# Performance work log

Measured on AMD Instinct MI355X. Metric: run time of the kernel, lower is better.

The kernel has to match this reference:

```python
import jax, jax.numpy as jnp
import numpy as np

K = 20
EPS = 1e-5


def _bn(x, g, b):
    # inference-mode BatchNorm with running_mean=0, running_var=1 (fresh init)
    return x * (g / jnp.sqrt(1.0 + EPS)) + b


def _lrelu(x):
    return jax.nn.leaky_relu(x, 0.2)


def _knn(x, k):
    # x: [B,N,D] -> idx [B,N,k] of nearest neighbors (includes self)
    sq = jnp.sum(x * x, axis=-1)                       # [B,N]
    inner = jnp.einsum('bnd,bmd->bnm', x, x)           # [B,N,N]
    dist = sq[:, :, None] - 2.0 * inner + sq[:, None, :]
    _, idx = jax.lax.top_k(-dist, k)
    return idx


def _edge_feat(x, k):
    # x: [B,N,D] -> [B,N,k,2D] = concat(neighbor - center, center)
    idx = _knn(x, k)
    nbr = jax.vmap(lambda xb, ib: xb[ib])(x, idx)      # [B,N,k,D]
    ctr = jnp.broadcast_to(x[:, :, None, :], nbr.shape)
    return jnp.concatenate([nbr - ctr, ctr], axis=-1)


def _edge_conv(x, W, g, b, k):
    # conv1x1 (no bias) + BN + LeakyReLU + max over neighbors
    f = _edge_feat(x, k)                               # [B,N,k,2D]
    h = jnp.einsum('bnkc,oc->bnko', f, W)
    return jnp.max(_lrelu(_bn(h, g, b)), axis=2)       # [B,N,out]


def setup_inputs() -> dict:
    key = jax.random.key(0)
    ks = jax.random.split(key, 12)
    B, N = 8, 4096
    num_classes = 5
    r = lambda k_, shape: jax.random.normal(k_, shape, jnp.float32) * 0.1
    return {
        'xyz': jax.random.normal(ks[0], (B, N, 3), jnp.float32),
        'W1': r(ks[1], (64, 6)),   'g1': jnp.ones((64,), jnp.float32),  'b1': jnp.zeros((64,), jnp.float32),
        'W2': r(ks[2], (64, 128)), 'g2': jnp.ones((64,), jnp.float32),  'b2': jnp.zeros((64,), jnp.float32),
        'W3': r(ks[3], (64, 128)), 'g3': jnp.ones((64,), jnp.float32),  'b3': jnp.zeros((64,), jnp.float32),
        'W4': r(ks[4], (128, 128)),'g4': jnp.ones((128,), jnp.float32), 'b4': jnp.zeros((128,), jnp.float32),
        'W5': r(ks[5], (1024, 320)),'g5': jnp.ones((1024,), jnp.float32),'b5': jnp.zeros((1024,), jnp.float32),
        'Wl1': r(ks[6], (512, 2048)),'g6': jnp.ones((512,), jnp.float32),'b6': jnp.zeros((512,), jnp.float32),
        'Wl2': r(ks[7], (256, 512)), 'bl2': jnp.zeros((256,), jnp.float32),
        'g7': jnp.ones((256,), jnp.float32), 'b7': jnp.zeros((256,), jnp.float32),
        'Wl3': r(ks[8], (num_classes, 256)), 'bl3': jnp.zeros((num_classes,), jnp.float32),
    }


def reference(xyz, W1, g1, b1, W2, g2, b2, W3, g3, b3, W4, g4, b4,
              W5, g5, b5, Wl1, g6, b6, Wl2, bl2, g7, b7, Wl3, bl3):
    B, N, _ = xyz.shape
    k = min(K, N - 1)
    x1 = _edge_conv(xyz, W1, g1, b1, k)                # [B,N,64]
    x2 = _edge_conv(x1, W2, g2, b2, k)                 # [B,N,64]
    x3 = _edge_conv(x2, W3, g3, b3, k)                 # [B,N,64]
    x4 = _edge_conv(x3, W4, g4, b4, k)                 # [B,N,128]
    xc = jnp.concatenate([x1, x2, x3, x4], axis=-1)    # [B,N,320]
    h = _lrelu(_bn(jnp.einsum('bnc,oc->bno', xc, W5), g5, b5))  # [B,N,1024]
    gmax = jnp.max(h, axis=1)
    gavg = jnp.mean(h, axis=1)
    gfeat = jnp.concatenate([gmax, gavg], axis=-1)     # [B,2048]
    y = _lrelu(_bn(gfeat @ Wl1.T, g6, b6))             # dropout = identity (eval)
    y = _lrelu(_bn(y @ Wl2.T + bl2, g7, b7))
    y = y @ Wl3.T + bl3                                # [B,num_classes]
    return jnp.broadcast_to(y[:, None, :], (B, N, y.shape[-1]))
```

## Files before the change

### kernel.cpp

```cpp
#include <hip/hip_runtime.h>


constexpr int NB  = 8;
constexpr int NPT = 4096;
constexpr int KNB = 20;

typedef _Float16 half8 __attribute__((ext_vector_type(8)));
typedef float f32x4 __attribute__((ext_vector_type(4)));

__device__ __forceinline__ unsigned int fmono(float f) {
  unsigned int u = __float_as_uint(f);
  return u ^ ((unsigned int)(((int)u) >> 31) | 0x80000000u);
}

__device__ __attribute__((noinline)) unsigned long long sort_row(int row, int n,
                                                                 int lane) {
  extern __shared__ char smem[];
  unsigned long long* buf = (unsigned long long*)smem + (size_t)row * 64;
  const unsigned long long INFK = ~0ull;
  unsigned long long a = (lane < n) ? buf[lane] : INFK;
#pragma unroll
  for (int k = 2; k <= 64; k <<= 1) {
#pragma unroll
    for (int j = k >> 1; j > 0; j >>= 1) {
      const bool tm = (((lane & k) == 0) == ((lane & j) == 0));
      const unsigned long long oa = __shfl_xor(a, j, 64);
      a = ((a < oa) == tm) ? a : oa;
    }
  }
  if (lane < 20) buf[lane] = a;
  return a;
}

__device__ __forceinline__ void sel_q(unsigned long long key, int base_r,
                                      int quad, int l15, int lane,
                                      unsigned long long& tau_r, int& cnt_r) {
  extern __shared__ char smem[];
  unsigned long long* bufB = (unsigned long long*)smem;
  bool pass = key < tau_r;
  unsigned long long m = __ballot(pass);
  if (m == 0) return;
  unsigned int seg = (unsigned int)(m >> (quad * 16)) & 0xFFFFu;
  int pc = __popc(seg);
  const unsigned long long needm = __ballot(cnt_r + pc > 64);
  if (needm != 0) {
#pragma unroll
    for (int q = 0; q < 4; ++q) {
      if ((needm >> (q * 16)) & 1ull) {
        const int nq = __shfl(cnt_r, q * 16, 64);
        const unsigned long long sv = sort_row(base_r + q * 4, nq, lane);
        const unsigned long long t19 = __shfl(sv, 19, 64);
        if (quad == q) { tau_r = t19; cnt_r = 20; }
      }
    }
    pass = key < tau_r;
    m = __ballot(pass);
    seg = (unsigned int)(m >> (quad * 16)) & 0xFFFFu;
    pc = __popc(seg);
  }
  if (pass) {
    const int off = __popc(seg & ((1u << l15) - 1u));
    bufB[(size_t)(base_r + quad * 4) * 64 + cnt_r + off] = key;
  }
  cnt_r += pc;
}

__global__ __launch_bounds__(256) void cvt_xyz(const float* __restrict__ xyz,
                                               float* __restrict__ x0) {
  const int t = blockIdx.x * 256 + threadIdx.x;
  float4 v;
  v.x = xyz[t * 3 + 0];
  v.y = xyz[t * 3 + 1];
  v.z = xyz[t * 3 + 2];
  v.w = 0.0f;
  *(float4*)(x0 + (size_t)t * 4) = v;
}

__global__ __launch_bounds__(256) void sqsplit(const float* __restrict__ x,
                                               float* __restrict__ sqo,
                                               unsigned short* __restrict__ xhi,
                                               unsigned short* __restrict__ xlo) {
  const int t = blockIdx.x * 256 + threadIdx.x;
  const int p = t >> 2, c = t & 3;
  const float* src = x + (size_t)p * 64 + c * 16;
  float s = 0.0f;
  unsigned short hb[16], lb[16];
#pragma unroll
  for (int e = 0; e < 16; e += 4) {
    const float4 v = *(const float4*)(src + e);
    const float vv[4] = {v.x, v.y, v.z, v.w};
#pragma unroll
    for (int u = 0; u < 4; ++u) {
      const float f = vv[u];
      s = fmaf(f, f, s);
      const _Float16 h = (_Float16)f;
      const _Float16 l = (_Float16)(f - (float)h);
      hb[e + u] = __builtin_bit_cast(unsigned short, h);
      lb[e + u] = __builtin_bit_cast(unsigned short, l);
    }
  }
  unsigned short* dh = xhi + (size_t)p * 64 + c * 16;
  unsigned short* dl = xlo + (size_t)p * 64 + c * 16;
  *(uint4*)dh = *(uint4*)hb;
  *(uint4*)(dh + 8) = *(uint4*)(hb + 8);
  *(uint4*)dl = *(uint4*)lb;
  *(uint4*)(dl + 8) = *(uint4*)(lb + 8);
  s += __shfl_xor(s, 1, 64);
  s += __shfl_xor(s, 2, 64);
  if (c == 0) sqo[p] = s;
}

__global__ __launch_bounds__(256, 4) void knn3(const float* __restrict__ x0,
                                               int* __restrict__ idxout) {
  const int b = blockIdx.y, i0 = blockIdx.x * 64;
  const int tid = threadIdx.x, w = tid >> 6, lane = tid & 63;
  const int l15 = lane & 15, quad = lane >> 4;
  const float* xb = x0 + (size_t)b * (NPT * 4);

  float xix[4], xiy[4], xiz[4];
#pragma unroll
  for (int r = 0; r < 4; ++r) {
    const float4 v =
        *(const float4*)(xb + (size_t)(i0 + w * 16 + quad * 4 + r) * 4);
    xix[r] = v.x;
    xiy[r] = v.y;
    xiz[r] = v.z;
  }

  unsigned long long tau[4] = {~0ull, ~0ull, ~0ull, ~0ull};
  int cnt[4] = {0, 0, 0, 0};

  for (int jt = 0; jt < NPT / 64; ++jt) {
    const int j0 = jt * 64;
    float4 xj[4];
#pragma unroll
    for (int nj = 0; nj < 4; ++nj)
      xj[nj] = *(const float4*)(xb + (size_t)(j0 + nj * 16 + l15) * 4);
#pragma unroll
    for (int r = 0; r < 4; ++r) {
#pragma unroll
      for (int nj = 0; nj < 4; ++nj) {
        const float dx = xj[nj].x - xix[r];
        const float dy = xj[nj].y - xiy[r];
        const float dz = xj[nj].z - xiz[r];
        const float dd = fmaf(dx, dx, fmaf(dy, dy, dz * dz));
        const unsigned long long key =
            ((unsigned long long)fmono(dd) << 32) |
            (unsigned int)(j0 + nj * 16 + l15);
        sel_q(key, w * 16 + r, quad, l15, lane, tau[r], cnt[r]);
      }
    }
  }
#pragma unroll
  for (int rw = 0; rw < 16; ++rw) {
    const int q = rw >> 2, r = rw & 3;
    const int nq = __shfl(cnt[r], q * 16, 64);
    const unsigned long long sv = sort_row(w * 16 + rw, nq, lane);
    const int i = i0 + w * 16 + rw;
    if (lane < 20)
      idxout[((size_t)(b * NPT + i)) * KNB + lane] = (int)(unsigned int)sv;
  }
}

__global__ __launch_bounds__(256, 4) void knn_mfma(
    const unsigned short* __restrict__ xhi16,
    const unsigned short* __restrict__ xlo16,
    const float* __restrict__ sqn, int* __restrict__ idxout) {
  const int b = blockIdx.y, i0 = blockIdx.x * 64;
  const int tid = threadIdx.x, w = tid >> 6, lane = tid & 63;
  const int l15 = lane & 15, quad = lane >> 4;

  const half8* Hb = (const half8*)(xhi16 + (size_t)b * NPT * 64);
  const half8* Lb = (const half8*)(xlo16 + (size_t)b * NPT * 64);
  const float* sqb = sqn + b * NPT;

  const int ia = i0 + w * 16 + l15;
  const half8 ah0 = Hb[(size_t)ia * 8 + quad];
  const half8 ah1 = Hb[(size_t)ia * 8 + 4 + quad];
  const half8 al0 = Lb[(size_t)ia * 8 + quad];
  const half8 al1 = Lb[(size_t)ia * 8 + 4 + quad];

  unsigned long long tau[4] = {~0ull, ~0ull, ~0ull, ~0ull};
  int cnt[4] = {0, 0, 0, 0};

  for (int jt = 0; jt < NPT / 64; ++jt) {
    const int j0 = jt * 64;
    float sq4[4];
#pragma unroll
    for (int nj = 0; nj < 4; ++nj) sq4[nj] = sqb[j0 + nj * 16 + l15];
    f32x4 acc[4];
#pragma unroll
    for (int nj = 0; nj < 4; ++nj) {
      const int jb = j0 + nj * 16 + l15;
      const half8 bh0 = Hb[(size_t)jb * 8 + quad];
      const half8 bh1 = Hb[(size_t)jb * 8 + 4 + quad];
      const half8 bl0 = Lb[(size_t)jb * 8 + quad];
      const half8 bl1 = Lb[(size_t)jb * 8 + 4 + quad];
      f32x4 a = {0.0f, 0.0f, 0.0f, 0.0f};
      a = __builtin_amdgcn_mfma_f32_16x16x32_f16(al0, bh0, a, 0, 0, 0);
      a = __builtin_amdgcn_mfma_f32_16x16x32_f16(al1, bh1, a, 0, 0, 0);
      a = __builtin_amdgcn_mfma_f32_16x16x32_f16(ah0, bl0, a, 0, 0, 0);
      a = __builtin_amdgcn_mfma_f32_16x16x32_f16(ah1, bl1, a, 0, 0, 0);
      a = __builtin_amdgcn_mfma_f32_16x16x32_f16(ah0, bh0, a, 0, 0, 0);
      a = __builtin_amdgcn_mfma_f32_16x16x32_f16(ah1, bh1, a, 0, 0, 0);
      acc[nj] = a;
    }
#pragma unroll
    for (int r = 0; r < 4; ++r) {
#pragma unroll
      for (int nj = 0; nj < 4; ++nj) {
        const float dd = fmaf(-2.0f, acc[nj][r], sq4[nj]);
        const unsigned long long key =
            ((unsigned long long)fmono(dd) << 32) |
            (unsigned int)(j0 + nj * 16 + l15);
        sel_q(key, w * 16 + r, quad, l15, lane, tau[r], cnt[r]);
      }
    }
  }
#pragma unroll
  for (int rw = 0; rw < 16; ++rw) {
    const int q = rw >> 2, r = rw & 3;
    const int nq = __shfl(cnt[r], q * 16, 64);
    const unsigned long long sv = sort_row(w * 16 + rw, nq, lane);
    const int i = i0 + w * 16 + rw;
    if (lane < 20)
      idxout[((size_t)(b * NPT + i)) * KNB + lane] = (int)(unsigned int)sv;
  }
}

__global__ __launch_bounds__(256) void featg3(const float* __restrict__ x0,
                                              const float* __restrict__ W,
                                              float* __restrict__ Y) {
  const int lane = threadIdx.x & 63;
  const int p0 = (blockIdx.x * 4 + (threadIdx.x >> 6)) * 4;
  const float* wr = W + lane * 6;
  const float w0 = wr[0], w1 = wr[1], w2 = wr[2];
#pragma unroll
  for (int r = 0; r < 4; ++r) {
    const float4 v = *(const float4*)(x0 + (size_t)(p0 + r) * 4);
    Y[(size_t)(p0 + r) * 64 + lane] = w0 * v.x + w1 * v.y + w2 * v.z;
  }
}

__global__ __launch_bounds__(256) void featg64(const float* __restrict__ X,
                                               const float* __restrict__ W,
                                               int co, float* __restrict__ Y) {
  __shared__ float Xt[64][68];
  __shared__ float Wt[64][68];
  const int tid = threadIdx.x;
  const int n0 = blockIdx.x * 64;
  const int pc = tid & 63, dg = tid >> 6;
#pragma unroll
  for (int rep = 0; rep < 4; ++rep) {
    const int d0 = dg * 16 + rep * 4;
    const float4 xv = *(const float4*)(X + (size_t)(n0 + pc) * 64 + d0);
    Xt[d0 + 0][pc] = xv.x; Xt[d0 + 1][pc] = xv.y;
    Xt[d0 + 2][pc] = xv.z; Xt[d0 + 3][pc] = xv.w;
    const float4 wv = *(const float4*)(W + (size_t)(co + pc) * 128 + d0);
    Wt[d0 + 0][pc] = wv.x; Wt[d0 + 1][pc] = wv.y;
    Wt[d0 + 2][pc] = wv.z; Wt[d0 + 3][pc] = wv.w;
  }
  __syncthreads();
  const int c0 = (tid & 15) * 4, p0 = (tid >> 4) * 4;
  float acc[4][4];
#pragma unroll
  for (int i = 0; i < 4; ++i)
#pragma unroll
    for (int j = 0; j < 4; ++j) acc[i][j] = 0.0f;
#pragma unroll 4
  for (int d = 0; d < 64; ++d) {
    const float4 xa = *(const float4*)&Xt[d][p0];
    const float4 wc = *(const float4*)&Wt[d][c0];
    const float xr[4] = {xa.x, xa.y, xa.z, xa.w};
    const float wr[4] = {wc.x, wc.y, wc.z, wc.w};
#pragma unroll
    for (int i = 0; i < 4; ++i)
#pragma unroll
      for (int j = 0; j < 4; ++j) acc[i][j] = fmaf(xr[i], wr[j], acc[i][j]);
  }
#pragma unroll
  for (int i = 0; i < 4; ++i) {
    float4 o;
    o.x = acc[i][0]; o.y = acc[i][1]; o.z = acc[i][2]; o.w = acc[i][3];
    *(float4*)(Y + (size_t)(n0 + p0 + i) * 64 + c0) = o;
  }
}

template <int DIN, int DS, int COUT>
__global__ __launch_bounds__(256) void gather_edge(
    const float* __restrict__ x, const float* __restrict__ Y,
    const int* __restrict__ idx, const float* __restrict__ W,
    const float* __restrict__ g, const float* __restrict__ bia,
    float* __restrict__ out, int co) {
  const int lane = threadIdx.x & 63;
  const int wglob = blockIdx.x * 4 + (threadIdx.x >> 6);
  const int b = wglob >> 12;
  const int c = co + lane;

  const float* wrow = W + (size_t)c * (2 * DIN);
  const float* xi = x + (size_t)wglob * DS;
  float Dv = 0.0f;
  if constexpr (DIN == 3) {
    const float4 v = *(const float4*)xi;
    Dv = (wrow[3] - wrow[0]) * v.x + (wrow[4] - wrow[1]) * v.y +
         (wrow[5] - wrow[2]) * v.z;
  } else {
#pragma unroll
    for (int d0 = 0; d0 < DIN; d0 += 4) {
      const float4 wa4 = *(const float4*)(wrow + d0);
      const float4 wb4 = *(const float4*)(wrow + DIN + d0);
      const float4 v = *(const float4*)(xi + d0);
      Dv += (wb4.x - wa4.x) * v.x + (wb4.y - wa4.y) * v.y +
            (wb4.z - wa4.z) * v.z + (wb4.w - wa4.w) * v.w;
    }
  }
  const float invs = 1.0f / sqrtf(1.0f + 1e-5f);
  const float s = g[c] * invs;
  const float base = fmaf(s, Dv, bia[c]);

  const int* ip = idx + (size_t)wglob * KNB;
  const int jv = ip[lane < KNB ? lane : 0];
  const float* Yb = Y + (((size_t)b) << 12) * 64;
  float m = -3.0e38f;
#pragma unroll
  for (int k = 0; k < KNB; ++k) {
    const int j = __shfl(jv, k, 64);
    const float yv = Yb[(size_t)j * 64 + lane];
    float v = fmaf(s, yv, base);
    v = v > 0.0f ? v : 0.2f * v;
    m = fmaxf(m, v);
  }
  out[(size_t)wglob * COUT + c] = m;
}

__global__ __launch_bounds__(256) void conv5_kernel(
    const float* __restrict__ x1, const float* __restrict__ x2,
    const float* __restrict__ x3, const float* __restrict__ x4,
    const float* __restrict__ W5, const float* __restrict__ g5,
    const float* __restrict__ b5, float* __restrict__ pmax,
    float* __restrict__ psum) {
  __shared__ float xcT[320][32];
  __shared__ float wT[8][256];
  const int nb = blockIdx.x, cb = blockIdx.y, b = blockIdx.z;
  const int tid = threadIdx.x;
  const int n0 = nb * 32;

#pragma unroll
  for (int p = 0; p < 10; ++p) {
    const int q = tid + p * 256;
    const int nloc = q / 80;
    const int kg = (q % 80) * 4;
    const float* src;
    int koff;
    if (kg < 64)       { src = x1 + ((size_t)(b * NPT + n0 + nloc)) * 64;  koff = kg; }
    else if (kg < 128) { src = x2 + ((size_t)(b * NPT + n0 + nloc)) * 64;  koff = kg - 64; }
    else if (kg < 192) { src = x3 + ((size_t)(b * NPT + n0 + nloc)) * 64;  koff = kg - 128; }
    else               { src = x4 + ((size_t)(b * NPT + n0 + nloc)) * 128; koff = kg - 192; }
    const float4 v = *(const float4*)(src + koff);
    xcT[kg + 0][nloc] = v.x; xcT[kg + 1][nloc] = v.y;
    xcT[kg + 2][nloc] = v.z; xcT[kg + 3][nloc] = v.w;
  }

  const int cg = tid >> 2, ng = tid & 3;
  const int c0 = cg * 4, n0t = ng * 8;
  float acc[4][8];
#pragma unroll
  for (int r = 0; r < 4; ++r)
#pragma unroll
    for (int e = 0; e < 8; ++e) acc[r][e] = 0.0f;

  for (int kt = 0; kt < 40; ++kt) {
    __syncthreads();
    {
      const float* wsrc = W5 + (size_t)(cb * 256 + tid) * 320 + kt * 8;
      const float4 a = *(const float4*)wsrc;
      const float4 b4 = *(const float4*)(wsrc + 4);
      wT[0][tid] = a.x; wT[1][tid] = a.y; wT[2][tid] = a.z; wT[3][tid] = a.w;
      wT[4][tid] = b4.x; wT[5][tid] = b4.y; wT[6][tid] = b4.z; wT[7][tid] = b4.w;
    }
    __syncthreads();
#pragma unroll
    for (int kk = 0; kk < 8; ++kk) {
      const float4 w4 = *(const float4*)&wT[kk][c0];
      const float4 xa = *(const float4*)&xcT[kt * 8 + kk][n0t];
      const float4 xb4 = *(const float4*)&xcT[kt * 8 + kk][n0t + 4];
      const float wr[4] = {w4.x, w4.y, w4.z, w4.w};
      const float xr[8] = {xa.x, xa.y, xa.z, xa.w, xb4.x, xb4.y, xb4.z, xb4.w};
#pragma unroll
      for (int r = 0; r < 4; ++r)
#pragma unroll
        for (int e = 0; e < 8; ++e) acc[r][e] = fmaf(wr[r], xr[e], acc[r][e]);
    }
  }

  const float invs = 1.0f / sqrtf(1.0f + 1e-5f);
#pragma unroll
  for (int r = 0; r < 4; ++r) {
    const int cglob = cb * 256 + c0 + r;
    const float s = g5[cglob] * invs;
    const float bb = b5[cglob];
    float mx = -3.0e38f, sm = 0.0f;
#pragma unroll
    for (int e = 0; e < 8; ++e) {
      float v = fmaf(s, acc[r][e], bb);
      v = v > 0.0f ? v : 0.2f * v;
      mx = fmaxf(mx, v);
      sm += v;
    }
    mx = fmaxf(mx, __shfl_xor(mx, 1, 64));
    mx = fmaxf(mx, __shfl_xor(mx, 2, 64));
    sm += __shfl_xor(sm, 1, 64);
    sm += __shfl_xor(sm, 2, 64);
    if (ng == 0) {
      pmax[((size_t)b * 1024 + cglob) * 128 + nb] = mx;
      psum[((size_t)b * 1024 + cglob) * 128 + nb] = sm;
    }
  }
}

__global__ __launch_bounds__(256) void reduce5(const float* __restrict__ pmax,
                                               const float* __restrict__ psum,
                                               float* __restrict__ gfeat) {
  const int t = blockIdx.x * 256 + threadIdx.x;
  const int b = t >> 10, c = t & 1023;
  const float* pm = pmax + (size_t)t * 128;
  const float* ps = psum + (size_t)t * 128;
  float mx = -3.0e38f, sm = 0.0f;
  for (int i = 0; i < 128; i += 4) {
    const float4 v = *(const float4*)(pm + i);
    mx = fmaxf(mx, fmaxf(fmaxf(v.x, v.y), fmaxf(v.z, v.w)));
    const float4 u = *(const float4*)(ps + i);
    sm += (u.x + u.y) + (u.z + u.w);
  }
  gfeat[b * 2048 + c] = mx;
  gfeat[b * 2048 + 1024 + c] = sm * (1.0f / 4096.0f);
}

__global__ __launch_bounds__(256) void head1(const float* __restrict__ gfeat,
                                             const float* __restrict__ Wl1,
                                             const float* __restrict__ g6,
                                             const float* __restrict__ b6,
                                             float* __restrict__ y1g) {
  __shared__ float gf[2048];
  __shared__ float red[256];
  const int tid = threadIdx.x;
  const int cb = blockIdx.x, b = blockIdx.y;
  const float4* gsrc = (const float4*)(gfeat + b * 2048);
  for (int p = tid; p < 512; p += 256) ((float4*)gf)[p] = gsrc[p];
  __syncthreads();
  const int cl = cb * 64 + (tid >> 2);
  const int q = tid & 3;
  const float* wr = Wl1 + (size_t)cl * 2048 + q * 512;
  const float* gq = gf + q * 512;
  float acc = 0.0f;
  for (int k0 = 0; k0 < 512; k0 += 8) {
    const float4 w0 = *(const float4*)(wr + k0);
    const float4 w1 = *(const float4*)(wr + k0 + 4);
    acc = fmaf(w0.x, gq[k0 + 0], acc); acc = fmaf(w0.y, gq[k0 + 1], acc);
    acc = fmaf(w0.z, gq[k0 + 2], acc); acc = fmaf(w0.w, gq[k0 + 3], acc);
    acc = fmaf(w1.x, gq[k0 + 4], acc); acc = fmaf(w1.y, gq[k0 + 5], acc);
    acc = fmaf(w1.z, gq[k0 + 6], acc); acc = fmaf(w1.w, gq[k0 + 7], acc);
  }
  red[tid] = acc;
  __syncthreads();
  if (q == 0) {
    float v = red[tid] + red[tid + 1] + red[tid + 2] + red[tid + 3];
    const float invs = 1.0f / sqrtf(1.0f + 1e-5f);
    v = fmaf(g6[cl] * invs, v, b6[cl]);
    v = v > 0.0f ? v : 0.2f * v;
    y1g[b * 512 + cl] = v;
  }
}

__global__ __launch_bounds__(256) void head2(
    const float* __restrict__ y1g, const float* __restrict__ Wl2,
    const float* __restrict__ bl2, const float* __restrict__ g7,
    const float* __restrict__ b7, const float* __restrict__ Wl3,
    const float* __restrict__ bl3, float* __restrict__ out) {
  __shared__ float y1s[512];
  __shared__ float y2s[256];
  __shared__ float y3s[5];
  const int b = blockIdx.x;
  const int t = threadIdx.x;
  y1s[t] = y1g[b * 512 + t];
  y1s[t + 256] = y1g[b * 512 + t + 256];
  __syncthreads();
  {
    const float* wr = Wl2 + (size_t)t * 512;
    float acc = 0.0f;
    for (int k0 = 0; k0 < 512; k0 += 8) {
      const float4 w0 = *(const float4*)(wr + k0);
      const float4 w1 = *(const float4*)(wr + k0 + 4);
      acc = fmaf(w0.x, y1s[k0 + 0], acc); acc = fmaf(w0.y, y1s[k0 + 1], acc);
      acc = fmaf(w0.z, y1s[k0 + 2], acc); acc = fmaf(w0.w, y1s[k0 + 3], acc);
      acc = fmaf(w1.x, y1s[k0 + 4], acc); acc = fmaf(w1.y, y1s[k0 + 5], acc);
      acc = fmaf(w1.z, y1s[k0 + 6], acc); acc = fmaf(w1.w, y1s[k0 + 7], acc);
    }
    const float invs = 1.0f / sqrtf(1.0f + 1e-5f);
    float v = acc + bl2[t];
    v = fmaf(g7[t] * invs, v, b7[t]);
    v = v > 0.0f ? v : 0.2f * v;
    y2s[t] = v;
  }
  __syncthreads();
  if (t < 5) {
    const float* wr = Wl3 + (size_t)t * 256;
    float acc = 0.0f;
    for (int k = 0; k < 256; ++k) acc += wr[k] * y2s[k];
    y3s[t] = acc + bl3[t];
  }
  __syncthreads();
  for (int e = t; e < NPT * 5; e += 256)
    out[(size_t)b * (NPT * 5) + e] = y3s[e % 5];
}

extern "C" void kernel_launch(void* const* d_in, const int* in_sizes, int n_in,
                              void* d_out, int out_size, void* d_ws, size_t ws_size,
                              hipStream_t stream) {
  (void)in_sizes; (void)n_in; (void)out_size;
  const float* xyz = (const float*)d_in[0];
  const float* W1  = (const float*)d_in[1];
  const float* g1  = (const float*)d_in[2];
  const float* b1  = (const float*)d_in[3];
  const float* W2  = (const float*)d_in[4];
  const float* g2  = (const float*)d_in[5];
  const float* b2  = (const float*)d_in[6];
  const float* W3  = (const float*)d_in[7];
  const float* g3  = (const float*)d_in[8];
  const float* b3  = (const float*)d_in[9];
  const float* W4  = (const float*)d_in[10];
  const float* g4  = (const float*)d_in[11];
  const float* b4  = (const float*)d_in[12];
  const float* W5  = (const float*)d_in[13];
  const float* g5  = (const float*)d_in[14];
  const float* b5  = (const float*)d_in[15];
  const float* Wl1 = (const float*)d_in[16];
  const float* g6  = (const float*)d_in[17];
  const float* b6  = (const float*)d_in[18];
  const float* Wl2 = (const float*)d_in[19];
  const float* bl2 = (const float*)d_in[20];
  const float* g7  = (const float*)d_in[21];
  const float* b7  = (const float*)d_in[22];
  const float* Wl3 = (const float*)d_in[23];
  const float* bl3 = (const float*)d_in[24];

  char* ws = (char*)d_ws;
  float* x0    = (float*)(ws + 0);
  float* x1    = (float*)(ws + 524288);
  float* x2    = (float*)(ws + 8912896);
  float* x3    = (float*)(ws + 17301504);
  float* x4    = (float*)(ws + 25690112);
  float* sqb   = (float*)(ws + 42467328);
  int*   idxb  = (int*)  (ws + 42598400);
  float* pmx   = (float*)(ws + 45219840);
  float* psm   = (float*)(ws + 49414144);
  float* gfeat = (float*)(ws + 53608448);
  float* y1g   = (float*)(ws + 53673984);
  if (ws_size < 53690368) return;

  unsigned short* xhi = (unsigned short*)pmx;
  unsigned short* xlo = (unsigned short*)psm;
  float* Yb = pmx;

  cvt_xyz<<<128, 256, 0, stream>>>(xyz, x0);

  knn3<<<dim3(64, 8), 256, 32768, stream>>>(x0, idxb);
  featg3<<<2048, 256, 0, stream>>>(x0, W1, Yb);
  gather_edge<3, 4, 64><<<8192, 256, 0, stream>>>(x0, Yb, idxb, W1, g1, b1, x1, 0);

  sqsplit<<<512, 256, 0, stream>>>(x1, sqb, xhi, xlo);
  knn_mfma<<<dim3(64, 8), 256, 32768, stream>>>(xhi, xlo, sqb, idxb);
  featg64<<<512, 256, 0, stream>>>(x1, W2, 0, Yb);
  gather_edge<64, 64, 64><<<8192, 256, 0, stream>>>(x1, Yb, idxb, W2, g2, b2, x2, 0);

  sqsplit<<<512, 256, 0, stream>>>(x2, sqb, xhi, xlo);
  knn_mfma<<<dim3(64, 8), 256, 32768, stream>>>(xhi, xlo, sqb, idxb);
  featg64<<<512, 256, 0, stream>>>(x2, W3, 0, Yb);
  gather_edge<64, 64, 64><<<8192, 256, 0, stream>>>(x2, Yb, idxb, W3, g3, b3, x3, 0);

  sqsplit<<<512, 256, 0, stream>>>(x3, sqb, xhi, xlo);
  knn_mfma<<<dim3(64, 8), 256, 32768, stream>>>(xhi, xlo, sqb, idxb);
  featg64<<<512, 256, 0, stream>>>(x3, W4, 0, Yb);
  gather_edge<64, 64, 128><<<8192, 256, 0, stream>>>(x3, Yb, idxb, W4, g4, b4, x4, 0);
  featg64<<<512, 256, 0, stream>>>(x3, W4, 64, Yb);
  gather_edge<64, 64, 128><<<8192, 256, 0, stream>>>(x3, Yb, idxb, W4, g4, b4, x4, 64);

  conv5_kernel<<<dim3(128, 4, 8), 256, 0, stream>>>(x1, x2, x3, x4, W5, g5, b5, pmx, psm);
  reduce5<<<32, 256, 0, stream>>>(pmx, psm, gfeat);
  head1<<<dim3(8, 8), 256, 0, stream>>>(gfeat, Wl1, g6, b6, y1g);
  head2<<<8, 256, 0, stream>>>(y1g, Wl2, bl2, g7, b7, Wl3, bl3, (float*)d_out);
}
```

Before: 2.290 ms.

## Split kNN candidate scan into two halves with a merge kernel

The kNN kernels now split the candidate range into two halves per query tile, doubling the grid from 512 to 1024 blocks. Each half writes its 20 sorted keys to a partial buffer (reusing the x4 workspace), and a new bitonic merge kernel picks the final 20. The goal is better GPU occupancy, since 512 blocks underfill the device. This costs an extra launch and extra global traffic for the partial buffer. Separately, conv5 now register-prefetches the next W5 slice while the current one is stored to shared memory.

```diff
diff --git a/kernel.cpp b/kernel.cpp
--- a/kernel.cpp
+++ b/kernel.cpp
@@ -110,9 +110,30 @@
   if (c == 0) sqo[p] = s;
 }
 
+__global__ __launch_bounds__(256) void knn_merge(
+    const unsigned long long* __restrict__ part, int* __restrict__ idxout) {
+  const int lane = threadIdx.x & 63;
+  const int p = blockIdx.x * 4 + (threadIdx.x >> 6);
+  unsigned long long a = (lane < 40) ? part[(size_t)p * 40 + lane] : ~0ull;
+#pragma unroll
+  for (int k = 2; k <= 64; k <<= 1) {
+#pragma unroll
+    for (int j = k >> 1; j > 0; j >>= 1) {
+      const bool tm = (((lane & k) == 0) == ((lane & j) == 0));
+      const unsigned long long oa = __shfl_xor(a, j, 64);
+      a = ((a < oa) == tm) ? a : oa;
+    }
+  }
+  if (lane < 20) idxout[(size_t)p * KNB + lane] = (int)(unsigned int)a;
+}
+
 __global__ __launch_bounds__(256, 4) void knn3(const float* __restrict__ x0,
-                                               int* __restrict__ idxout) {
-  const int b = blockIdx.y, i0 = blockIdx.x * 64;
+                                               unsigned long long* __restrict__ part) {
+  const int bid = blockIdx.x;
+  const int b = bid & 7;
+  const int tb = bid >> 3;
+  const int i0 = (tb >> 1) * 64;
+  const int jh = tb & 1;
   const int tid = threadIdx.x, w = tid >> 6, lane = tid & 63;
   const int l15 = lane & 15, quad = lane >> 4;
   const float* xb = x0 + (size_t)b * (NPT * 4);
@@ -130,7 +151,7 @@
   unsigned long long tau[4] = {~0ull, ~0ull, ~0ull, ~0ull};
   int cnt[4] = {0, 0, 0, 0};
 
-  for (int jt = 0; jt < NPT / 64; ++jt) {
+  for (int jt = jh * 32; jt < jh * 32 + 32; ++jt) {
     const int j0 = jt * 64;
     float4 xj[4];
 #pragma unroll
@@ -158,15 +179,19 @@
     const unsigned long long sv = sort_row(w * 16 + rw, nq, lane);
     const int i = i0 + w * 16 + rw;
     if (lane < 20)
-      idxout[((size_t)(b * NPT + i)) * KNB + lane] = (int)(unsigned int)sv;
+      part[((size_t)(b * NPT + i)) * 40 + jh * 20 + lane] = sv;
   }
 }
 
 __global__ __launch_bounds__(256, 4) void knn_mfma(
     const unsigned short* __restrict__ xhi16,
     const unsigned short* __restrict__ xlo16,
-    const float* __restrict__ sqn, int* __restrict__ idxout) {
-  const int b = blockIdx.y, i0 = blockIdx.x * 64;
+    const float* __restrict__ sqn, unsigned long long* __restrict__ part) {
+  const int bid = blockIdx.x;
+  const int b = bid & 7;
+  const int tb = bid >> 3;
+  const int i0 = (tb >> 1) * 64;
+  const int jh = tb & 1;
   const int tid = threadIdx.x, w = tid >> 6, lane = tid & 63;
   const int l15 = lane & 15, quad = lane >> 4;
 
@@ -183,7 +208,7 @@
   unsigned long long tau[4] = {~0ull, ~0ull, ~0ull, ~0ull};
   int cnt[4] = {0, 0, 0, 0};
 
-  for (int jt = 0; jt < NPT / 64; ++jt) {
+  for (int jt = jh * 32; jt < jh * 32 + 32; ++jt) {
     const int j0 = jt * 64;
     float sq4[4];
 #pragma unroll
@@ -224,7 +249,7 @@
     const unsigned long long sv = sort_row(w * 16 + rw, nq, lane);
     const int i = i0 + w * 16 + rw;
     if (lane < 20)
-      idxout[((size_t)(b * NPT + i)) * KNB + lane] = (int)(unsigned int)sv;
+      part[((size_t)(b * NPT + i)) * 40 + jh * 20 + lane] = sv;
   }
 }
 
@@ -369,15 +394,17 @@
 #pragma unroll
     for (int e = 0; e < 8; ++e) acc[r][e] = 0.0f;
 
+  const float* wbase = W5 + (size_t)(cb * 256 + tid) * 320;
+  float4 wA = *(const float4*)(wbase);
+  float4 wB = *(const float4*)(wbase + 4);
+
   for (int kt = 0; kt < 40; ++kt) {
     __syncthreads();
-    {
-      const float* wsrc = W5 + (size_t)(cb * 256 + tid) * 320 + kt * 8;
-      const float4 a = *(const float4*)wsrc;
-      const float4 b4 = *(const float4*)(wsrc + 4);
-      wT[0][tid] = a.x; wT[1][tid] = a.y; wT[2][tid] = a.z; wT[3][tid] = a.w;
-      wT[4][tid] = b4.x; wT[5][tid] = b4.y; wT[6][tid] = b4.z; wT[7][tid] = b4.w;
-    }
+    wT[0][tid] = wA.x; wT[1][tid] = wA.y; wT[2][tid] = wA.z; wT[3][tid] = wA.w;
+    wT[4][tid] = wB.x; wT[5][tid] = wB.y; wT[6][tid] = wB.z; wT[7][tid] = wB.w;
+    const int kn = (kt + 1 < 40) ? kt + 1 : 39;
+    float4 nA = *(const float4*)(wbase + kn * 8);
+    float4 nB = *(const float4*)(wbase + kn * 8 + 4);
     __syncthreads();
 #pragma unroll
     for (int kk = 0; kk < 8; ++kk) {
@@ -391,6 +418,7 @@
 #pragma unroll
         for (int e = 0; e < 8; ++e) acc[r][e] = fmaf(wr[r], xr[e], acc[r][e]);
     }
+    wA = nA; wB = nB;
   }
 
   const float invs = 1.0f / sqrtf(1.0f + 1e-5f);
@@ -561,25 +589,30 @@
   unsigned short* xhi = (unsigned short*)pmx;
   unsigned short* xlo = (unsigned short*)psm;
   float* Yb = pmx;
+  unsigned long long* part = (unsigned long long*)x4;
 
   cvt_xyz<<<128, 256, 0, stream>>>(xyz, x0);
 
-  knn3<<<dim3(64, 8), 256, 32768, stream>>>(x0, idxb);
+  knn3<<<1024, 256, 32768, stream>>>(x0, part);
+  knn_merge<<<8192, 256, 0, stream>>>(part, idxb);
   featg3<<<2048, 256, 0, stream>>>(x0, W1, Yb);
   gather_edge<3, 4, 64><<<8192, 256, 0, stream>>>(x0, Yb, idxb, W1, g1, b1, x1, 0);
 
   sqsplit<<<512, 256, 0, stream>>>(x1, sqb, xhi, xlo);
-  knn_mfma<<<dim3(64, 8), 256, 32768, stream>>>(xhi, xlo, sqb, idxb);
+  knn_mfma<<<1024, 256, 32768, stream>>>(xhi, xlo, sqb, part);
+  knn_merge<<<8192, 256, 0, stream>>>(part, idxb);
   featg64<<<512, 256, 0, stream>>>(x1, W2, 0, Yb);
   gather_edge<64, 64, 64><<<8192, 256, 0, stream>>>(x1, Yb, idxb, W2, g2, b2, x2, 0);
 
   sqsplit<<<512, 256, 0, stream>>>(x2, sqb, xhi, xlo);
-  knn_mfma<<<dim3(64, 8), 256, 32768, stream>>>(xhi, xlo, sqb, idxb);
+  knn_mfma<<<1024, 256, 32768, stream>>>(xhi, xlo, sqb, part);
+  knn_merge<<<8192, 256, 0, stream>>>(part, idxb);
   featg64<<<512, 256, 0, stream>>>(x2, W3, 0, Yb);
   gather_edge<64, 64, 64><<<8192, 256, 0, stream>>>(x2, Yb, idxb, W3, g3, b3, x3, 0);
 
   sqsplit<<<512, 256, 0, stream>>>(x3, sqb, xhi, xlo);
-  knn_mfma<<<dim3(64, 8), 256, 32768, stream>>>(xhi, xlo, sqb, idxb);
+  knn_mfma<<<1024, 256, 32768, stream>>>(xhi, xlo, sqb, part);
+  knn_merge<<<8192, 256, 0, stream>>>(part, idxb);
   featg64<<<512, 256, 0, stream>>>(x3, W4, 0, Yb);
   gather_edge<64, 64, 128><<<8192, 256, 0, stream>>>(x3, Yb, idxb, W4, g4, b4, x4, 0);
   featg64<<<512, 256, 0, stream>>>(x3, W4, 64, Yb);
```

Result: no change. 2.297 ms (+0.3%).

## Batch kNN candidate selection four keys at a time with larger 128-slot buffers

Applied to the files above, without the earlier changes.

The per-key ballot/compact selection in the kNN kernels is replaced by a four-key batched filter. It appends survivors to per-row candidate buffers enlarged to 128 entries. Compaction now runs a 128-element bitonic merge less often and writes back only the top 20, which cuts shuffle and ballot overhead per candidate. Shared memory doubles to 64 KB, with occupancy hints lowered to 2 blocks, a flattened batch-interleaved grid, and register prefetch of the next W5 tile in conv5.

```diff
diff --git a/kernel.cpp b/kernel.cpp
--- a/kernel.cpp
+++ b/kernel.cpp
@@ -4,6 +4,7 @@
 constexpr int NB  = 8;
 constexpr int NPT = 4096;
 constexpr int KNB = 20;
+constexpr int CAP = 128;
 
 typedef _Float16 half8 __attribute__((ext_vector_type(8)));
 typedef float f32x4 __attribute__((ext_vector_type(4)));
@@ -13,12 +14,13 @@
   return u ^ ((unsigned int)(((int)u) >> 31) | 0x80000000u);
 }
 
-__device__ __attribute__((noinline)) unsigned long long sort_row(int row, int n,
-                                                                 int lane) {
+__device__ __attribute__((noinline)) unsigned long long compact_row(
+    int row, int n, int lane) {
   extern __shared__ char smem[];
-  unsigned long long* buf = (unsigned long long*)smem + (size_t)row * 64;
+  unsigned long long* buf = (unsigned long long*)smem + (size_t)row * CAP;
   const unsigned long long INFK = ~0ull;
   unsigned long long a = (lane < n) ? buf[lane] : INFK;
+  unsigned long long c = (lane + 64 < n) ? buf[lane + 64] : INFK;
 #pragma unroll
   for (int k = 2; k <= 64; k <<= 1) {
 #pragma unroll
@@ -26,43 +28,65 @@
       const bool tm = (((lane & k) == 0) == ((lane & j) == 0));
       const unsigned long long oa = __shfl_xor(a, j, 64);
       a = ((a < oa) == tm) ? a : oa;
-    }
-  }
-  if (lane < 20) buf[lane] = a;
-  return a;
-}
-
-__device__ __forceinline__ void sel_q(unsigned long long key, int base_r,
-                                      int quad, int l15, int lane,
-                                      unsigned long long& tau_r, int& cnt_r) {
+      const unsigned long long oc = __shfl_xor(c, j, 64);
+      c = ((c < oc) == tm) ? oc : c;
+    }
+  }
+  unsigned long long m = a < c ? a : c;
+#pragma unroll
+  for (int j = 32; j > 0; j >>= 1) {
+    const unsigned long long o = __shfl_xor(m, j, 64);
+    const bool low = (lane & j) == 0;
+    m = ((m < o) == low) ? m : o;
+  }
+  return m;
+}
+
+__device__ __forceinline__ void sel4(unsigned long long k0,
+                                     unsigned long long k1,
+                                     unsigned long long k2,
+                                     unsigned long long k3, int base_r,
+                                     int quad, int lane, unsigned int below,
+                                     unsigned long long& tau, int& cnt) {
   extern __shared__ char smem[];
   unsigned long long* bufB = (unsigned long long*)smem;
-  bool pass = key < tau_r;
-  unsigned long long m = __ballot(pass);
-  if (m == 0) return;
-  unsigned int seg = (unsigned int)(m >> (quad * 16)) & 0xFFFFu;
-  int pc = __popc(seg);
-  const unsigned long long needm = __ballot(cnt_r + pc > 64);
-  if (needm != 0) {
-#pragma unroll
-    for (int q = 0; q < 4; ++q) {
-      if ((needm >> (q * 16)) & 1ull) {
-        const int nq = __shfl(cnt_r, q * 16, 64);
-        const unsigned long long sv = sort_row(base_r + q * 4, nq, lane);
-        const unsigned long long t19 = __shfl(sv, 19, 64);
-        if (quad == q) { tau_r = t19; cnt_r = 20; }
+#pragma unroll 1
+  for (int attempt = 0; attempt < 2; ++attempt) {
+    const unsigned long long m0 = __ballot(k0 < tau);
+    const unsigned long long m1 = __ballot(k1 < tau);
+    const unsigned long long m2 = __ballot(k2 < tau);
+    const unsigned long long m3 = __ballot(k3 < tau);
+    if ((m0 | m1 | m2 | m3) == 0ull) return;
+    const int sh = quad * 16;
+    const unsigned int s0 = (unsigned int)(m0 >> sh) & 0xFFFFu;
+    const unsigned int s1 = (unsigned int)(m1 >> sh) & 0xFFFFu;
+    const unsigned int s2 = (unsigned int)(m2 >> sh) & 0xFFFFu;
+    const unsigned int s3 = (unsigned int)(m3 >> sh) & 0xFFFFu;
+    const int tot = __popc(s0) + __popc(s1) + __popc(s2) + __popc(s3);
+    const unsigned long long needm = __ballot(cnt + tot > CAP);
+    if (needm != 0ull && attempt == 0) {
+#pragma unroll
+      for (int q = 0; q < 4; ++q) {
+        if ((needm >> (q * 16)) & 1ull) {
+          const int nq = __shfl(cnt, q * 16, 64);
+          const unsigned long long sv = compact_row(base_r + q * 4, nq, lane);
+          const unsigned long long t19 = __shfl(sv, 19, 64);
+          if (lane < 20) bufB[(size_t)(base_r + q * 4) * CAP + lane] = sv;
+          if (quad == q) { tau = t19; cnt = 20; }
+        }
       }
-    }
-    pass = key < tau_r;
-    m = __ballot(pass);
-    seg = (unsigned int)(m >> (quad * 16)) & 0xFFFFu;
-    pc = __popc(seg);
-  }
-  if (pass) {
-    const int off = __popc(seg & ((1u << l15) - 1u));
-    bufB[(size_t)(base_r + quad * 4) * 64 + cnt_r + off] = key;
-  }
-  cnt_r += pc;
+      continue;
+    }
+    int pos = cnt + __popc(s0 & below) + __popc(s1 & below) +
+              __popc(s2 & below) + __popc(s3 & below);
+    unsigned long long* bp = bufB + (size_t)(base_r + quad * 4) * CAP;
+    if (k0 < tau) { bp[pos] = k0; ++pos; }
+    if (k1 < tau) { bp[pos] = k1; ++pos; }
+    if (k2 < tau) { bp[pos] = k2; ++pos; }
+    if (k3 < tau) { bp[pos] = k3; }
+    cnt += tot;
+    return;
+  }
 }
 
 __global__ __launch_bounds__(256) void cvt_xyz(const float* __restrict__ xyz,
@@ -110,11 +134,14 @@
   if (c == 0) sqo[p] = s;
 }
 
-__global__ __launch_bounds__(256, 4) void knn3(const float* __restrict__ x0,
+__global__ __launch_bounds__(256, 2) void knn3(const float* __restrict__ x0,
                                                int* __restrict__ idxout) {
-  const int b = blockIdx.y, i0 = blockIdx.x * 64;
+  const int bid = blockIdx.x;
+  const int b = bid & 7;
+  const int i0 = (bid >> 3) * 64;
   const int tid = threadIdx.x, w = tid >> 6, lane = tid & 63;
   const int l15 = lane & 15, quad = lane >> 4;
+  const unsigned int below = (1u << l15) - 1u;
   const float* xb = x0 + (size_t)b * (NPT * 4);
 
   float xix[4], xiy[4], xiz[4];
@@ -138,37 +165,41 @@
       xj[nj] = *(const float4*)(xb + (size_t)(j0 + nj * 16 + l15) * 4);
 #pragma unroll
     for (int r = 0; r < 4; ++r) {
+      unsigned long long k[4];
 #pragma unroll
       for (int nj = 0; nj < 4; ++nj) {
         const float dx = xj[nj].x - xix[r];
         const float dy = xj[nj].y - xiy[r];
         const float dz = xj[nj].z - xiz[r];
         const float dd = fmaf(dx, dx, fmaf(dy, dy, dz * dz));
-        const unsigned long long key =
-            ((unsigned long long)fmono(dd) << 32) |
-            (unsigned int)(j0 + nj * 16 + l15);
-        sel_q(key, w * 16 + r, quad, l15, lane, tau[r], cnt[r]);
+        k[nj] = ((unsigned long long)fmono(dd) << 32) |
+                (unsigned int)(j0 + nj * 16 + l15);
       }
-    }
-  }
-#pragma unroll
+      sel4(k[0], k[1], k[2], k[3], w * 16 + r, quad, lane, below, tau[r],
+           cnt[r]);
+    }
+  }
+#pragma unroll 1
   for (int rw = 0; rw < 16; ++rw) {
     const int q = rw >> 2, r = rw & 3;
     const int nq = __shfl(cnt[r], q * 16, 64);
-    const unsigned long long sv = sort_row(w * 16 + rw, nq, lane);
+    const unsigned long long sv = compact_row(w * 16 + rw, nq, lane);
     const int i = i0 + w * 16 + rw;
     if (lane < 20)
       idxout[((size_t)(b * NPT + i)) * KNB + lane] = (int)(unsigned int)sv;
   }
 }
 
-__global__ __launch_bounds__(256, 4) void knn_mfma(
+__global__ __launch_bounds__(256, 2) void knn_mfma(
     const unsigned short* __restrict__ xhi16,
     const unsigned short* __restrict__ xlo16,
     const float* __restrict__ sqn, int* __restrict__ idxout) {
-  const int b = blockIdx.y, i0 = blockIdx.x * 64;
+  const int bid = blockIdx.x;
+  const int b = bid & 7;
+  const int i0 = (bid >> 3) * 64;
   const int tid = threadIdx.x, w = tid >> 6, lane = tid & 63;
   const int l15 = lane & 15, quad = lane >> 4;
+  const unsigned int below = (1u << l15) - 1u;
 
   const half8* Hb = (const half8*)(xhi16 + (size_t)b * NPT * 64);
   const half8* Lb = (const half8*)(xlo16 + (size_t)b * NPT * 64);
@@ -207,21 +238,22 @@
     }
 #pragma unroll
     for (int r = 0; r < 4; ++r) {
+      unsigned long long k[4];
 #pragma unroll
       for (int nj = 0; nj < 4; ++nj) {
         const float dd = fmaf(-2.0f, acc[nj][r], sq4[nj]);
-        const unsigned long long key =
-            ((unsigned long long)fmono(dd) << 32) |
-            (unsigned int)(j0 + nj * 16 + l15);
-        sel_q(key, w * 16 + r, quad, l15, lane, tau[r], cnt[r]);
+        k[nj] = ((unsigned long long)fmono(dd) << 32) |
+                (unsigned int)(j0 + nj * 16 + l15);
       }
-    }
-  }
-#pragma unroll
+      sel4(k[0], k[1], k[2], k[3], w * 16 + r, quad, lane, below, tau[r],
+           cnt[r]);
+    }
+  }
+#pragma unroll 1
   for (int rw = 0; rw < 16; ++rw) {
     const int q = rw >> 2, r = rw & 3;
     const int nq = __shfl(cnt[r], q * 16, 64);
-    const unsigned long long sv = sort_row(w * 16 + rw, nq, lane);
+    const unsigned long long sv = compact_row(w * 16 + rw, nq, lane);
     const int i = i0 + w * 16 + rw;
     if (lane < 20)
       idxout[((size_t)(b * NPT + i)) * KNB + lane] = (int)(unsigned int)sv;
@@ -369,15 +401,17 @@
 #pragma unroll
     for (int e = 0; e < 8; ++e) acc[r][e] = 0.0f;
 
+  const float* wbase = W5 + (size_t)(cb * 256 + tid) * 320;
+  float4 wA = *(const float4*)(wbase);
+  float4 wB = *(const float4*)(wbase + 4);
+
   for (int kt = 0; kt < 40; ++kt) {
     __syncthreads();
-    {
-      const float* wsrc = W5 + (size_t)(cb * 256 + tid) * 320 + kt * 8;
-      const float4 a = *(const float4*)wsrc;
-      const float4 b4 = *(const float4*)(wsrc + 4);
-      wT[0][tid] = a.x; wT[1][tid] = a.y; wT[2][tid] = a.z; wT[3][tid] = a.w;
-      wT[4][tid] = b4.x; wT[5][tid] = b4.y; wT[6][tid] = b4.z; wT[7][tid] = b4.w;
-    }
+    wT[0][tid] = wA.x; wT[1][tid] = wA.y; wT[2][tid] = wA.z; wT[3][tid] = wA.w;
+    wT[4][tid] = wB.x; wT[5][tid] = wB.y; wT[6][tid] = wB.z; wT[7][tid] = wB.w;
+    const int kn = (kt + 1 < 40) ? kt + 1 : 39;
+    float4 nA = *(const float4*)(wbase + kn * 8);
+    float4 nB = *(const float4*)(wbase + kn * 8 + 4);
     __syncthreads();
 #pragma unroll
     for (int kk = 0; kk < 8; ++kk) {
@@ -391,6 +425,7 @@
 #pragma unroll
         for (int e = 0; e < 8; ++e) acc[r][e] = fmaf(wr[r], xr[e], acc[r][e]);
     }
+    wA = nA; wB = nB;
   }
 
   const float invs = 1.0f / sqrtf(1.0f + 1e-5f);
@@ -564,22 +599,22 @@
 
   cvt_xyz<<<128, 256, 0, stream>>>(xyz, x0);
 
-  knn3<<<dim3(64, 8), 256, 32768, stream>>>(x0, idxb);
+  knn3<<<512, 256, 65536, stream>>>(x0, idxb);
   featg3<<<2048, 256, 0, stream>>>(x0, W1, Yb);
   gather_edge<3, 4, 64><<<8192, 256, 0, stream>>>(x0, Yb, idxb, W1, g1, b1, x1, 0);
 
   sqsplit<<<512, 256, 0, stream>>>(x1, sqb, xhi, xlo);
-  knn_mfma<<<dim3(64, 8), 256, 32768, stream>>>(xhi, xlo, sqb, idxb);
+  knn_mfma<<<512, 256, 65536, stream>>>(xhi, xlo, sqb, idxb);
   featg64<<<512, 256, 0, stream>>>(x1, W2, 0, Yb);
   gather_edge<64, 64, 64><<<8192, 256, 0, stream>>>(x1, Yb, idxb, W2, g2, b2, x2, 0);
 
   sqsplit<<<512, 256, 0, stream>>>(x2, sqb, xhi, xlo);
-  knn_mfma<<<dim3(64, 8), 256, 32768, stream>>>(xhi, xlo, sqb, idxb);
+  knn_mfma<<<512, 256, 65536, stream>>>(xhi, xlo, sqb, idxb);
   featg64<<<512, 256, 0, stream>>>(x2, W3, 0, Yb);
   gather_edge<64, 64, 64><<<8192, 256, 0, stream>>>(x2, Yb, idxb, W3, g3, b3, x3, 0);
 
   sqsplit<<<512, 256, 0, stream>>>(x3, sqb, xhi, xlo);
-  knn_mfma<<<dim3(64, 8), 256, 32768, stream>>>(xhi, xlo, sqb, idxb);
+  knn_mfma<<<512, 256, 65536, stream>>>(xhi, xlo, sqb, idxb);
   featg64<<<512, 256, 0, stream>>>(x3, W4, 0, Yb);
   gather_edge<64, 64, 128><<<8192, 256, 0, stream>>>(x3, Yb, idxb, W4, g4, b4, x4, 0);
   featg64<<<512, 256, 0, stream>>>(x3, W4, 64, Yb);
```

After: 2.316 ms. No clear change (+1.1%).
